# Kernel optimization log

Hardware: AMD Instinct MI355X
Metric: run time of the kernel (lower is better)

## Reference

```python
import jax, jax.numpy as jnp
import numpy as np

B, N, F = 4096, 64, 128   # batch, max_neighbor, input feature dim
H, D = 8, 64              # num_heads, weight_dims (per head)
HD = H * D


def setup_inputs() -> dict:
    key = jax.random.key(0)
    k1, k2, k3, k4 = jax.random.split(key, 4)
    x = jax.random.normal(k1, (B, N, F), dtype=jnp.float32)
    W_lin = jax.random.normal(k2, (F, HD), dtype=jnp.float32) * (1.0 / np.sqrt(F))
    W_att = jax.random.normal(k3, (2 * HD, H), dtype=jnp.float32) * (1.0 / np.sqrt(2 * HD))
    mask = jax.random.randint(k4, (B, N), 0, 2, dtype=jnp.int32)
    return {"x": x, "W_lin": W_lin, "W_att": W_att, "mask": mask}


def reference(x, W_lin, W_att, mask):
    # dropout is identity (rate 0.0 / inference)
    lin = x @ W_lin                               # [B, N, H*D]
    # src node is neighbor slot 0 of each batch row (the Python-loop gather+tile)
    src = lin[:, 0, :]                            # [B, H*D]
    # attention_layer on concat([src, lin]) == src@W_att[:HD] + lin@W_att[HD:]
    att = src @ W_att[:HD]                        # [B, H]
    att = att[:, None, :] + lin @ W_att[HD:]      # [B, N, H]
    att = jnp.where(att >= 0, att, 0.2 * att)     # LeakyReLU(alpha=0.2)
    aw = jnp.transpose(att, (0, 2, 1))            # [B, H, N]  (split heads + squeeze)
    aw = aw + (mask == 0).astype(jnp.float32)[:, None, :] * (-1e9)
    aw = jax.nn.softmax(aw, axis=2)[..., None]    # [B, H, N, 1]
    lp = jnp.transpose(lin.reshape(B, N, H, D), (0, 2, 1, 3))  # [B, H, N, D]
    weighted = lp * aw                            # [B, H, N, D]
    # fusion 'concat': unstack heads, concat along last -> [B, N, H*D], then ReLU
    out = jnp.transpose(weighted, (0, 2, 1, 3)).reshape(B, N, HD)
    return jax.nn.relu(out)
```

## Files before the change

### kernel.cpp

```cpp
#include <hip/hip_runtime.h>


typedef _Float16 half8 __attribute__((ext_vector_type(8)));
typedef _Float16 half4v __attribute__((ext_vector_type(4)));
typedef float f32x4 __attribute__((ext_vector_type(4)));

static constexpr int NSEQ  = 64;
static constexpr int FIN   = 128;
static constexpr int HDIM  = 512;
static constexpr int NHEAD = 8;
static constexpr int LIN_LD = 520;
static constexpr int XS_LD  = 136;

__global__ __launch_bounds__(256) void prep_kernel(const float* __restrict__ wlin,
                                                   const float* __restrict__ watt,
                                                   _Float16* __restrict__ wlinT,
                                                   _Float16* __restrict__ wacat)
{
    int t = blockIdx.x * 256 + threadIdx.x;
    if (t < HDIM * FIN) {
        int c = t >> 7;
        int k = t & 127;
        wlinT[t] = (_Float16)wlin[k * HDIM + c];
    }
    if (t < 16 * HDIM) {
        int col = t >> 9;
        int k = t & 511;
        float v = (col < NHEAD) ? watt[(HDIM + k) * NHEAD + col]
                                : watt[k * NHEAD + (col - NHEAD)];
        wacat[t] = (_Float16)v;
    }
}

__global__ __launch_bounds__(512, 4) void fused_kernel(const float* __restrict__ x,
                                                       const _Float16* __restrict__ wlinT,
                                                       const _Float16* __restrict__ wacat,
                                                       const int* __restrict__ mask,
                                                       float* __restrict__ out)
{
    __shared__ _Float16 lin_s[NSEQ * LIN_LD];
    __shared__ float attbuf[2 * NSEQ * 17];
    __shared__ float aw_s[NSEQ * NHEAD];

    const int b    = blockIdx.x;
    const int t    = threadIdx.x;
    const int lane = t & 63;
    const int w    = t >> 6;
    const int l15  = lane & 15;
    const int quad = lane >> 4;

    _Float16* xs = lin_s;

    const f32x4* xb = (const f32x4*)(x + (size_t)b * (NSEQ * FIN));
    #pragma unroll
    for (int it = 0; it < 4; ++it) {
        int i = it * 512 + t;
        f32x4 v = __builtin_nontemporal_load(&xb[i]);
        int n = i >> 5;
        int k = (i & 31) << 2;
        half4v hv;
        hv[0] = (_Float16)v[0]; hv[1] = (_Float16)v[1];
        hv[2] = (_Float16)v[2]; hv[3] = (_Float16)v[3];
        *(half4v*)(xs + n * XS_LD + k) = hv;
    }
    __syncthreads();

    f32x4 acc[4][4];
    #pragma unroll
    for (int mt = 0; mt < 4; ++mt)
        #pragma unroll
        for (int nt = 0; nt < 4; ++nt)
            acc[mt][nt] = (f32x4){0.f, 0.f, 0.f, 0.f};

    const int colbase = w * 64;
    #pragma unroll
    for (int ks = 0; ks < 4; ++ks) {
        const int k0 = ks * 32 + quad * 8;
        half8 a[4];
        #pragma unroll
        for (int mt = 0; mt < 4; ++mt)
            a[mt] = *(const half8*)(wlinT + (colbase + mt * 16 + l15) * FIN + k0);
        #pragma unroll
        for (int nt = 0; nt < 4; ++nt) {
            half8 bfr = *(const half8*)(xs + (nt * 16 + l15) * XS_LD + k0);
            #pragma unroll
            for (int mt = 0; mt < 4; ++mt)
                acc[mt][nt] = __builtin_amdgcn_mfma_f32_16x16x32_f16(a[mt], bfr, acc[mt][nt], 0, 0, 0);
        }
    }
    __syncthreads();

    #pragma unroll
    for (int mt = 0; mt < 4; ++mt)
        #pragma unroll
        for (int nt = 0; nt < 4; ++nt) {
            half4v hv;
            #pragma unroll
            for (int i = 0; i < 4; ++i) hv[i] = (_Float16)acc[mt][nt][i];
            *(half4v*)(lin_s + (nt * 16 + l15) * LIN_LD + colbase + mt * 16 + quad * 4) = hv;
        }
    __syncthreads();

    {
        const int rt = w & 3;
        const int kh = w >> 2;
        f32x4 acca = (f32x4){0.f, 0.f, 0.f, 0.f};
        #pragma unroll
        for (int ks = 0; ks < 8; ++ks) {
            int k0 = kh * 256 + ks * 32 + quad * 8;
            half8 af = *(const half8*)(lin_s + (rt * 16 + l15) * LIN_LD + k0);
            half8 bf = *(const half8*)(wacat + l15 * HDIM + k0);
            acca = __builtin_amdgcn_mfma_f32_16x16x32_f16(af, bf, acca, 0, 0, 0);
        }
        #pragma unroll
        for (int i = 0; i < 4; ++i)
            attbuf[kh * NSEQ * 17 + (rt * 16 + quad * 4 + i) * 17 + l15] = acca[i];
    }
    __syncthreads();

    {
        const int mv = mask[b * NSEQ + lane];
        const float pen = (mv == 0) ? -1e9f : 0.0f;
        const int h = w;
        float srcv = attbuf[8 + h] + attbuf[NSEQ * 17 + 8 + h];
        float a = attbuf[lane * 17 + h] + attbuf[NSEQ * 17 + lane * 17 + h] + srcv;
        a = (a >= 0.0f) ? a : 0.2f * a;
        a += pen;
        float mx = a;
        #pragma unroll
        for (int off = 32; off > 0; off >>= 1)
            mx = fmaxf(mx, __shfl_xor(mx, off, 64));
        float e = __expf(a - mx);
        float s = e;
        #pragma unroll
        for (int off = 32; off > 0; off >>= 1)
            s += __shfl_xor(s, off, 64);
        aw_s[lane * NHEAD + h] = e / s;
    }
    __syncthreads();

    f32x4* ob = (f32x4*)(out + (size_t)b * (NSEQ * HDIM));
    #pragma unroll
    for (int it = 0; it < 16; ++it) {
        int i = it * 512 + t;
        int n = i >> 7;
        int c = (i & 127) << 2;
        float wgt = aw_s[n * NHEAD + (c >> 6)];
        half4v lv = *(const half4v*)(lin_s + n * LIN_LD + c);
        f32x4 o;
        o[0] = fmaxf((float)lv[0] * wgt, 0.0f);
        o[1] = fmaxf((float)lv[1] * wgt, 0.0f);
        o[2] = fmaxf((float)lv[2] * wgt, 0.0f);
        o[3] = fmaxf((float)lv[3] * wgt, 0.0f);
        __builtin_nontemporal_store(o, &ob[i]);
    }
}

extern "C" void kernel_launch(void* const* d_in, const int* in_sizes, int n_in,
                              void* d_out, int out_size, void* d_ws, size_t ws_size,
                              hipStream_t stream)
{
    const float* x    = (const float*)d_in[0];
    const float* wlin = (const float*)d_in[1];
    const float* watt = (const float*)d_in[2];
    const int*   mask = (const int*)d_in[3];
    float* out = (float*)d_out;

    _Float16* wlinT = (_Float16*)d_ws;
    _Float16* wacat = wlinT + HDIM * FIN;

    const int B = in_sizes[0] / (NSEQ * FIN);

    prep_kernel<<<256, 256, 0, stream>>>(wlin, watt, wlinT, wacat);
    fused_kernel<<<B, 512, 0, stream>>>(x, wlinT, wacat, mask, out);
}
```

Baseline: 648.0 us.

## Keep linear output in registers; compute attention logits from accumulators

Removes the half-precision lin tile from LDS. The attention projection is now computed directly from the MFMA accumulators using 16x16x16 MFMAs, with W_att prepacked in the operand layout. Per-wave partial logits are reduced through a small LDS buffer, and the output is written from registers via a per-wave LDS transpose. This cuts shared memory from about 80KB to about 39KB for higher occupancy and avoids the fp16 round trip of lin, at the cost of an extra reduction pass and a sync.

Result: no change. 639.4 us (-1.3%).

```diff
diff --git a/kernel.cpp b/kernel.cpp
--- a/kernel.cpp
+++ b/kernel.cpp
@@ -1,21 +1,22 @@
 #include <hip/hip_runtime.h>
 
 
-typedef _Float16 half8 __attribute__((ext_vector_type(8)));
+typedef _Float16 half8  __attribute__((ext_vector_type(8)));
 typedef _Float16 half4v __attribute__((ext_vector_type(4)));
-typedef float f32x4 __attribute__((ext_vector_type(4)));
+typedef float    f32x4  __attribute__((ext_vector_type(4)));
 
 static constexpr int NSEQ  = 64;
 static constexpr int FIN   = 128;
 static constexpr int HDIM  = 512;
 static constexpr int NHEAD = 8;
-static constexpr int LIN_LD = 520;
-static constexpr int XS_LD  = 136;
+static constexpr int XS_LD = 136;
+
+static constexpr int SMEM_BYTES = 39168;
 
 __global__ __launch_bounds__(256) void prep_kernel(const float* __restrict__ wlin,
                                                    const float* __restrict__ watt,
                                                    _Float16* __restrict__ wlinT,
-                                                   _Float16* __restrict__ wacat)
+                                                   _Float16* __restrict__ waA)
 {
     int t = blockIdx.x * 256 + threadIdx.x;
     if (t < HDIM * FIN) {
@@ -24,23 +25,27 @@
         wlinT[t] = (_Float16)wlin[k * HDIM + c];
     }
     if (t < 16 * HDIM) {
-        int col = t >> 9;
-        int k = t & 511;
-        float v = (col < NHEAD) ? watt[(HDIM + k) * NHEAD + col]
-                                : watt[k * NHEAD + (col - NHEAD)];
-        wacat[t] = (_Float16)v;
+        int i     = t & 3;
+        int lane  = (t >> 2) & 63;
+        int slice = t >> 8;
+        int c = (slice >> 2) * 64 + (slice & 3) * 16 + (lane >> 4) * 4 + i;
+        int j = lane & 15;
+        float v = (j < NHEAD) ? watt[(HDIM + c) * NHEAD + j]
+                              : watt[c * NHEAD + (j - NHEAD)];
+        waA[t] = (_Float16)v;
     }
 }
 
 __global__ __launch_bounds__(512, 4) void fused_kernel(const float* __restrict__ x,
                                                        const _Float16* __restrict__ wlinT,
-                                                       const _Float16* __restrict__ wacat,
+                                                       const _Float16* __restrict__ waA,
                                                        const int* __restrict__ mask,
                                                        float* __restrict__ out)
 {
-    __shared__ _Float16 lin_s[NSEQ * LIN_LD];
-    __shared__ float attbuf[2 * NSEQ * 17];
-    __shared__ float aw_s[NSEQ * NHEAD];
+    __shared__ char smem[SMEM_BYTES] __attribute__((aligned(16)));
+    _Float16* xs     = (_Float16*)smem;
+    float*    attbuf = (float*)smem;
+    float*    att_s  = (float*)(smem + 34816);
 
     const int b    = blockIdx.x;
     const int t    = threadIdx.x;
@@ -49,7 +54,7 @@
     const int l15  = lane & 15;
     const int quad = lane >> 4;
 
-    _Float16* xs = lin_s;
+    const int mv = mask[b * NSEQ + lane];
 
     const f32x4* xb = (const f32x4*)(x + (size_t)b * (NSEQ * FIN));
     #pragma unroll
@@ -90,40 +95,45 @@
     }
     __syncthreads();
 
-    #pragma unroll
-    for (int mt = 0; mt < 4; ++mt)
+    {
+        f32x4 T[4];
         #pragma unroll
-        for (int nt = 0; nt < 4; ++nt) {
-            half4v hv;
+        for (int nt = 0; nt < 4; ++nt) T[nt] = (f32x4){0.f, 0.f, 0.f, 0.f};
+        #pragma unroll
+        for (int mt = 0; mt < 4; ++mt) {
+            half4v aF = *(const half4v*)(waA + ((w * 4 + mt) * 64 + lane) * 4);
             #pragma unroll
-            for (int i = 0; i < 4; ++i) hv[i] = (_Float16)acc[mt][nt][i];
-            *(half4v*)(lin_s + (nt * 16 + l15) * LIN_LD + colbase + mt * 16 + quad * 4) = hv;
-        }
-    __syncthreads();
-
-    {
-        const int rt = w & 3;
-        const int kh = w >> 2;
-        f32x4 acca = (f32x4){0.f, 0.f, 0.f, 0.f};
-        #pragma unroll
-        for (int ks = 0; ks < 8; ++ks) {
-            int k0 = kh * 256 + ks * 32 + quad * 8;
-            half8 af = *(const half8*)(lin_s + (rt * 16 + l15) * LIN_LD + k0);
-            half8 bf = *(const half8*)(wacat + l15 * HDIM + k0);
-            acca = __builtin_amdgcn_mfma_f32_16x16x32_f16(af, bf, acca, 0, 0, 0);
+            for (int nt = 0; nt < 4; ++nt) {
+                half4v bF;
+                #pragma unroll
+                for (int i = 0; i < 4; ++i) bF[i] = (_Float16)acc[mt][nt][i];
+                T[nt] = __builtin_amdgcn_mfma_f32_16x16x16f16(aF, bF, T[nt], 0, 0, 0);
+            }
         }
         #pragma unroll
-        for (int i = 0; i < 4; ++i)
-            attbuf[kh * NSEQ * 17 + (rt * 16 + quad * 4 + i) * 17 + l15] = acca[i];
+        for (int nt = 0; nt < 4; ++nt)
+            *(f32x4*)(attbuf + (w * 64 + nt * 16 + l15) * 16 + quad * 4) = T[nt];
     }
     __syncthreads();
 
     {
-        const int mv = mask[b * NSEQ + lane];
+        int n  = t >> 3;
+        int j0 = (t & 7) * 2;
+        float s0 = 0.f, s1 = 0.f;
+        #pragma unroll
+        for (int ww = 0; ww < 8; ++ww) {
+            const float* p = attbuf + (ww * 64 + n) * 16 + j0;
+            s0 += p[0]; s1 += p[1];
+        }
+        att_s[n * 17 + j0]     = s0;
+        att_s[n * 17 + j0 + 1] = s1;
+    }
+    __syncthreads();
+
+    float aw_reg;
+    {
         const float pen = (mv == 0) ? -1e9f : 0.0f;
-        const int h = w;
-        float srcv = attbuf[8 + h] + attbuf[NSEQ * 17 + 8 + h];
-        float a = attbuf[lane * 17 + h] + attbuf[NSEQ * 17 + lane * 17 + h] + srcv;
+        float a = att_s[lane * 17 + w] + att_s[8 + w];
         a = (a >= 0.0f) ? a : 0.2f * a;
         a += pen;
         float mx = a;
@@ -135,24 +145,31 @@
         #pragma unroll
         for (int off = 32; off > 0; off >>= 1)
             s += __shfl_xor(s, off, 64);
-        aw_s[lane * NHEAD + h] = e / s;
+        aw_reg = e / s;
     }
-    __syncthreads();
 
-    f32x4* ob = (f32x4*)(out + (size_t)b * (NSEQ * HDIM));
-    #pragma unroll
-    for (int it = 0; it < 16; ++it) {
-        int i = it * 512 + t;
-        int n = i >> 7;
-        int c = (i & 127) << 2;
-        float wgt = aw_s[n * NHEAD + (c >> 6)];
-        half4v lv = *(const half4v*)(lin_s + n * LIN_LD + c);
-        f32x4 o;
-        o[0] = fmaxf((float)lv[0] * wgt, 0.0f);
-        o[1] = fmaxf((float)lv[1] * wgt, 0.0f);
-        o[2] = fmaxf((float)lv[2] * wgt, 0.0f);
-        o[3] = fmaxf((float)lv[3] * wgt, 0.0f);
-        __builtin_nontemporal_store(o, &ob[i]);
+    {
+        float* ft = (float*)smem + w * (16 * 68);
+        float* outb = out + (size_t)b * (NSEQ * HDIM);
+        #pragma unroll
+        for (int nt = 0; nt < 4; ++nt) {
+            float awv = __shfl(aw_reg, nt * 16 + l15, 64);
+            #pragma unroll
+            for (int mt = 0; mt < 4; ++mt) {
+                f32x4 o;
+                #pragma unroll
+                for (int i = 0; i < 4; ++i)
+                    o[i] = fmaxf(acc[mt][nt][i] * awv, 0.0f);
+                *(f32x4*)(ft + l15 * 68 + mt * 16 + quad * 4) = o;
+            }
+            #pragma unroll
+            for (int s = 0; s < 4; ++s) {
+                int r = s * 4 + quad;
+                f32x4 v = *(const f32x4*)(ft + r * 68 + l15 * 4);
+                int n = nt * 16 + r;
+                __builtin_nontemporal_store(v, (f32x4*)(outb + n * HDIM + w * 64 + l15 * 4));
+            }
+        }
     }
 }
 
@@ -167,10 +184,10 @@
     float* out = (float*)d_out;
 
     _Float16* wlinT = (_Float16*)d_ws;
-    _Float16* wacat = wlinT + HDIM * FIN;
+    _Float16* waA   = wlinT + HDIM * FIN;
 
     const int B = in_sizes[0] / (NSEQ * FIN);
 
-    prep_kernel<<<256, 256, 0, stream>>>(wlin, watt, wlinT, wacat);
-    fused_kernel<<<B, 512, 0, stream>>>(x, wlinT, wacat, mask, out);
+    prep_kernel<<<256, 256, 0, stream>>>(wlin, watt, wlinT, waA);
+    fused_kernel<<<B, 512, 0, stream>>>(x, wlinT, waA, mask, out);
 }
```
